# Performance work log

Hardware: AMD Instinct MI355X
Metric: run time of the kernel (lower is better)

The kernel has to match this reference:

```python
import jax, jax.numpy as jnp
import numpy as np

B, S, E, H = 2, 2048, 1024, 16
D = E // H  # head_dim = 64


def _rope_angles(seq_len, d, dtype=jnp.float32):
    # standard RoPE frequencies: theta_i = 10000^{-2i/d}
    inv_freq = 1.0 / (10000.0 ** (jnp.arange(0, d, 2, dtype=dtype) / d))  # [d/2]
    pos = jnp.arange(seq_len, dtype=dtype)                                # [S]
    ang = pos[:, None] * inv_freq[None, :]                                # [S, d/2]
    ang = jnp.concatenate([ang, ang], axis=-1)                            # [S, d]
    return jnp.cos(ang), jnp.sin(ang)


def _rotate_half(t):
    t1, t2 = jnp.split(t, 2, axis=-1)
    return jnp.concatenate([-t2, t1], axis=-1)


def _apply_rope(t, cos, sin):
    # t: [B, H, S, D]; cos/sin: [S, D]
    return t * cos[None, None, :, :] + _rotate_half(t) * sin[None, None, :, :]


def setup_inputs() -> dict:
    key = jax.random.key(0)
    ks = jax.random.split(key, 6)
    x = jax.random.normal(ks[0], (B, S, E), dtype=jnp.float32)
    mask = jnp.tril(jnp.ones((S, S), dtype=bool))  # causal: True = attend
    scale = 1.0 / np.sqrt(E)
    Wq = jax.random.normal(ks[1], (E, E), dtype=jnp.float32) * scale
    Wk = jax.random.normal(ks[2], (E, E), dtype=jnp.float32) * scale
    Wv = jax.random.normal(ks[3], (E, E), dtype=jnp.float32) * scale
    Wo = jax.random.normal(ks[4], (E, E), dtype=jnp.float32) * scale
    z = jnp.zeros((E,), dtype=jnp.float32)
    return {"x": x, "mask": mask, "Wq": Wq, "bq": z, "Wk": Wk, "bk": z,
            "Wv": Wv, "bv": z, "Wo": Wo, "bo": z}


def reference(x, mask, Wq, bq, Wk, bk, Wv, bv, Wo, bo):
    b, s, e = x.shape
    # QKV projections (nn.Linear convention: y = x @ W.T + b)
    def proj(W, bias):
        y = jnp.einsum('bse,fe->bsf', x, W) + bias
        return y.reshape(b, s, H, D).transpose(0, 2, 1, 3)  # [B,H,S,D]
    q, k, v = proj(Wq, bq), proj(Wk, bk), proj(Wv, bv)
    # RoPE on q and k (per-head rotary over head_dim)
    cos, sin = _rope_angles(s, D, dtype=x.dtype)
    q = _apply_rope(q, cos, sin)
    k = _apply_rope(k, cos, sin)
    # SDPA with boolean mask (True = attend)
    scores = jnp.einsum('bhqd,bhkd->bhqk', q, k) / jnp.sqrt(jnp.asarray(D, x.dtype))
    neg = jnp.asarray(jnp.finfo(x.dtype).min, x.dtype)
    scores = jnp.where(mask[None, None, :, :], scores, neg)
    attn = jax.nn.softmax(scores, axis=-1)
    out = jnp.einsum('bhqk,bhkd->bhqd', attn, v)          # [B,H,S,D]
    out = out.transpose(0, 2, 1, 3).reshape(b, s, e)       # [B,S,E]
    return jnp.einsum('bse,fe->bsf', out, Wo) + bo
```

## Files before the change

### kernel.cpp

```cpp
#include <hip/hip_runtime.h>
#include <hip/hip_bf16.h>

typedef unsigned short u16;
typedef unsigned int u32;
typedef __bf16 bf16x8 __attribute__((ext_vector_type(8)));
typedef float f32x4 __attribute__((ext_vector_type(4)));

#define S_LEN 2048
#define NHEAD 16
#define HDIM  64
#define EMB   1024
#define BATCH 2

__device__ __forceinline__ float bf2f(u16 u) {
  union { unsigned int i; float f; } c; c.i = ((unsigned int)u) << 16; return c.f;
}
__device__ __forceinline__ u16 f2bf(float f) {
  union { float f; unsigned int i; } c; c.f = f;
  unsigned int i = c.i;
  return (u16)((i + 0x7FFFu + ((i >> 16) & 1u)) >> 16);
}
__device__ __forceinline__ u16 f2bf_trunc(float f) {
  union { float f; unsigned int i; } c; c.f = f;
  return (u16)(c.i >> 16);
}
__device__ __forceinline__ f32x4 mfma16(bf16x8 a, bf16x8 b, f32x4 c) {
  return __builtin_amdgcn_mfma_f32_16x16x32_bf16(a, b, c, 0, 0, 0);
}
__device__ __forceinline__ void cp16(const u16* g, u16* l) {
  __builtin_amdgcn_global_load_lds(
      (const __attribute__((address_space(1))) u32*)g,
      (__attribute__((address_space(3))) u32*)l, 16, 0, 0);
}

__global__ __launch_bounds__(256) void convert_kernel(
    const void* __restrict__ x, const void* __restrict__ Wq,
    const void* __restrict__ Wk, const void* __restrict__ Wv,
    const void* __restrict__ Wo,
    u16* __restrict__ xb, u16* __restrict__ wqb, u16* __restrict__ wkb,
    u16* __restrict__ wvb, u16* __restrict__ wob,
    int* __restrict__ flag, float2* __restrict__ tab)
{
  __shared__ int s_flag;
  if (threadIdx.x == 0) s_flag = 0;
  __syncthreads();
  {
    const u16* xs = (const u16*)x;
    u16 w0 = xs[threadIdx.x * 2], w1 = xs[threadIdx.x * 2 + 1];
    if ((((w0 >> 7) & 0xFF) >= 0xC0) || (((w1 >> 7) & 0xFF) >= 0xC0))
      atomicOr(&s_flag, 1);
  }
  __syncthreads();
  const int f32io = s_flag;
  if (blockIdx.x == 0 && threadIdx.x == 0) flag[0] = f32io;

  size_t gid = (size_t)blockIdx.x * 256 + threadIdx.x;
  size_t e = gid * 8;
  const void* src; u16* dst; size_t off;
  if (e < 4194304) { src = x; dst = xb; off = e; }
  else {
    size_t rr = e - 4194304;
    int j = (int)(rr >> 20); off = rr & 1048575;
    src = (j == 0) ? Wq : (j == 1) ? Wk : (j == 2) ? Wv : Wo;
    dst = (j == 0) ? wqb : (j == 1) ? wkb : (j == 2) ? wvb : wob;
  }
  if (f32io) {
    const float* s = (const float*)src + off;
    float4 a = *(const float4*)s;
    float4 b2 = *(const float4*)(s + 4);
    ushort4 u0; u0.x = f2bf(a.x); u0.y = f2bf(a.y); u0.z = f2bf(a.z); u0.w = f2bf(a.w);
    ushort4 u1; u1.x = f2bf(b2.x); u1.y = f2bf(b2.y); u1.z = f2bf(b2.z); u1.w = f2bf(b2.w);
    *(ushort4*)(dst + off) = u0;
    *(ushort4*)(dst + off + 4) = u1;
  } else {
    *(uint4*)(dst + off) = *(const uint4*)((const u16*)src + off);
  }

  if (blockIdx.x < 256) {
    int id = blockIdx.x * 256 + threadIdx.x;
    int s = id >> 5, i = id & 31;
    float f = exp2f(-(float)i * 0.41524101186092029f);
    float ang = (float)s * f;
    tab[id] = make_float2(cosf(ang), sinf(ang));
  }
}

__device__ __forceinline__ void gemm_core_db(
    const u16* __restrict__ A, const u16* __restrict__ W,
    int m0, int n0, int t, f32x4 (&acc)[4][4],
    u16* __restrict__ Ash, u16* __restrict__ Bsh)
{
  const int lane = t & 63, lr = lane & 15, quad = lane >> 4;
  const int wv = t >> 6;
  const int wm = (wv & 1) * 64, wn = (wv >> 1) * 64;
  const int r0 = t >> 2;
  const int r1 = (t + 256) >> 2;
  const int c0 = (((t & 3) ^ ((t >> 2) & 3))) * 8;
  const int lds0 = (t & 192) * 8;
  const int lds1 = (256 + (t & 192)) * 8;
  const int qx = ((quad ^ (lr & 3))) * 8;
  const u16* gA0 = A + (size_t)(m0 + r0) * 1024 + c0;
  const u16* gA1 = A + (size_t)(m0 + r1) * 1024 + c0;
  const u16* gB0 = W + (size_t)(n0 + r0) * 1024 + c0;
  const u16* gB1 = W + (size_t)(n0 + r1) * 1024 + c0;

  cp16(gA0, Ash + lds0); cp16(gA1, Ash + lds1);
  cp16(gB0, Bsh + lds0); cp16(gB1, Bsh + lds1);
  __syncthreads();

  for (int kt = 0; kt < 1024; kt += 32) {
    const int cur = (kt >> 5) & 1;
    const u16* Ac = Ash + cur * 4096;
    const u16* Bc = Bsh + cur * 4096;
    bf16x8 af[4], bfr[4];
#pragma unroll
    for (int mi = 0; mi < 4; ++mi)
      af[mi] = *(const bf16x8*)(Ac + (wm + mi * 16 + lr) * 32 + qx);
#pragma unroll
    for (int ni = 0; ni < 4; ++ni)
      bfr[ni] = *(const bf16x8*)(Bc + (wn + ni * 16 + lr) * 32 + qx);
    if (kt + 32 < 1024) {
      u16* An = Ash + (1 - cur) * 4096;
      u16* Bn = Bsh + (1 - cur) * 4096;
      cp16(gA0 + kt + 32, An + lds0); cp16(gA1 + kt + 32, An + lds1);
      cp16(gB0 + kt + 32, Bn + lds0); cp16(gB1 + kt + 32, Bn + lds1);
    }
#pragma unroll
    for (int mi = 0; mi < 4; ++mi)
#pragma unroll
      for (int ni = 0; ni < 4; ++ni)
        acc[mi][ni] = mfma16(af[mi], bfr[ni], acc[mi][ni]);
    __syncthreads();
  }
}

__device__ __forceinline__ void gemm_epilogue(
    int mode, int f32io, f32x4 (&acc)[4][4],
    const void* biasvp, void* outvp, int m0, int n0, int t,
    const float2* __restrict__ tab)
{
  const int lane = t & 63, lr = lane & 15, quad = lane >> 4;
  const int wv = t >> 6;
  const int wm = (wv & 1) * 64, wn = (wv >> 1) * 64;
  const float* biasf = (const float*)biasvp;
  const u16* biasb = (const u16*)biasvp;
#define BIASV(n) (f32io ? biasf[(n)] : bf2f(biasb[(n)]))
  if (mode == 1) {
    u16* Out = (u16*)outvp;
#pragma unroll
    for (int mi = 0; mi < 4; ++mi) {
#pragma unroll
      for (int r = 0; r < 4; ++r) {
        int mm = m0 + wm + mi * 16 + quad * 4 + r;
        int s = mm & (S_LEN - 1), b = mm >> 11;
        float2 cs0 = tab[s * 32 + lr];
        float2 cs1 = tab[s * 32 + 16 + lr];
#pragma unroll
        for (int ni = 0; ni < 4; ++ni) {
          int n = n0 + wn + ni * 16 + lr;
          int h = n >> 6, d = n & 63;
          float v  = acc[mi][ni][r]     + BIASV(n);
          float vp = acc[mi][ni ^ 2][r] + BIASV(n ^ 32);
          float rot = (d < 32) ? -vp : vp;
          float cc = (ni & 1) ? cs1.x : cs0.x;
          float ss = (ni & 1) ? cs1.y : cs0.y;
          size_t off = (((size_t)(b * NHEAD + h)) * S_LEN + s) * HDIM + d;
          Out[off] = f2bf(v * cc + rot * ss);
        }
      }
    }
  } else if (mode == 2) {
    u16* Out = (u16*)outvp;
#pragma unroll
    for (int mi = 0; mi < 4; ++mi) {
      int mm = m0 + wm + mi * 16 + quad * 4;
      int s = mm & (S_LEN - 1), b = mm >> 11;
#pragma unroll
      for (int ni = 0; ni < 4; ++ni) {
        int n = n0 + wn + ni * 16 + lr;
        int h = n >> 6, d = n & 63;
        float bv = BIASV(n);
        u16 p0 = f2bf(acc[mi][ni][0] + bv);
        u16 p1 = f2bf(acc[mi][ni][1] + bv);
        u16 p2 = f2bf(acc[mi][ni][2] + bv);
        u16 p3 = f2bf(acc[mi][ni][3] + bv);
        uint2 pk = make_uint2((u32)p0 | ((u32)p1 << 16),
                              (u32)p2 | ((u32)p3 << 16));
        size_t off = (((size_t)(b * NHEAD + h)) * HDIM + d) * S_LEN + s;
        *(uint2*)(Out + off) = pk;
      }
    }
  }
#undef BIASV
}

__global__ __launch_bounds__(256) void gemm_qkv(
    const u16* __restrict__ A, const u16* __restrict__ Wq,
    const u16* __restrict__ Wk, const u16* __restrict__ Wv,
    const void* bq, const void* bk, const void* bv,
    u16* qo, u16* ko, u16* vo, const int* __restrict__ dflag,
    const float2* __restrict__ tab)
{
  alignas(16) __shared__ u16 Ash[2 * 128 * 32];
  alignas(16) __shared__ u16 Bsh[2 * 128 * 32];
  const int lin = blockIdx.y * 24 + blockIdx.x;
  const int xcd = lin & 7, rr = lin >> 3;
  const int mt = (xcd << 2) + (rr & 3);
  const int nw = rr >> 2;
  const int wsel = nw >> 3;
  const u16* W = (wsel == 0) ? Wq : (wsel == 1) ? Wk : Wv;
  const void* bias = (wsel == 0) ? bq : (wsel == 1) ? bk : bv;
  void* out = (wsel == 0) ? (void*)qo : (wsel == 1) ? (void*)ko : (void*)vo;
  const int mode = (wsel == 2) ? 2 : 1;
  const int m0 = mt * 128, n0 = (nw & 7) * 128;
  f32x4 acc[4][4];
  const f32x4 zero4 = {0.f, 0.f, 0.f, 0.f};
#pragma unroll
  for (int i = 0; i < 4; ++i)
#pragma unroll
    for (int j = 0; j < 4; ++j) acc[i][j] = zero4;
  gemm_core_db(A, W, m0, n0, threadIdx.x, acc, Ash, Bsh);
  gemm_epilogue(mode, dflag[0], acc, bias, out, m0, n0, threadIdx.x, tab);
}

__global__ __launch_bounds__(256) void gemm_out(
    const u16* __restrict__ A, const u16* __restrict__ W,
    const void* bias, void* out, const int* __restrict__ dflag)
{
  alignas(16) __shared__ u16 Ash[2 * 64 * 32];
  alignas(16) __shared__ u16 Bsh[2 * 128 * 32];
  const int t = threadIdx.x, lane = t & 63, wv = t >> 6;
  const int lr = lane & 15, quad = lane >> 4;
  const int lin = blockIdx.y * 8 + blockIdx.x;
  const int xcd = lin & 7, rl = lin >> 3;
  const int mt = (xcd << 3) + (rl & 7);
  const int m0 = mt * 64, n0 = (rl >> 3) * 128;
  const int wm = (wv & 1) * 32, wn = (wv >> 1) * 64;
  const int f32io = dflag[0];

  const int r0 = t >> 2;
  const int r1 = (t + 256) >> 2;
  const int c0 = (((t & 3) ^ ((t >> 2) & 3))) * 8;
  const int lds0 = (t & 192) * 8;
  const int lds1 = (256 + (t & 192)) * 8;
  const int qx = ((quad ^ (lr & 3))) * 8;
  const u16* gA0 = A + (size_t)(m0 + (r0 & 63)) * 1024 + c0;
  const u16* gB0 = W + (size_t)(n0 + r0) * 1024 + c0;
  const u16* gB1 = W + (size_t)(n0 + r1) * 1024 + c0;

  f32x4 acc[2][4];
  const f32x4 zero4 = {0.f, 0.f, 0.f, 0.f};
#pragma unroll
  for (int i = 0; i < 2; ++i)
#pragma unroll
    for (int j = 0; j < 4; ++j) acc[i][j] = zero4;

  cp16(gA0, Ash + lds0);
  cp16(gB0, Bsh + lds0); cp16(gB1, Bsh + lds1);
  __syncthreads();

  for (int kt = 0; kt < 1024; kt += 32) {
    const int cur = (kt >> 5) & 1;
    const u16* Ac = Ash + cur * 2048;
    const u16* Bc = Bsh + cur * 4096;
    bf16x8 af[2], bfr[4];
#pragma unroll
    for (int mi = 0; mi < 2; ++mi)
      af[mi] = *(const bf16x8*)(Ac + (wm + mi * 16 + lr) * 32 + qx);
#pragma unroll
    for (int ni = 0; ni < 4; ++ni)
      bfr[ni] = *(const bf16x8*)(Bc + (wn + ni * 16 + lr) * 32 + qx);
    if (kt + 32 < 1024) {
      u16* An = Ash + (1 - cur) * 2048;
      u16* Bn = Bsh + (1 - cur) * 4096;
      cp16(gA0 + kt + 32, An + lds0);
      cp16(gB0 + kt + 32, Bn + lds0); cp16(gB1 + kt + 32, Bn + lds1);
    }
#pragma unroll
    for (int mi = 0; mi < 2; ++mi)
#pragma unroll
      for (int ni = 0; ni < 4; ++ni)
        acc[mi][ni] = mfma16(af[mi], bfr[ni], acc[mi][ni]);
    __syncthreads();
  }

  const float* biasf = (const float*)bias;
  const u16* biasb = (const u16*)bias;
  float* Outf = (float*)out;
  u16* Outb = (u16*)out;
#pragma unroll
  for (int mi = 0; mi < 2; ++mi) {
#pragma unroll
    for (int r = 0; r < 4; ++r) {
      int mm = m0 + wm + mi * 16 + quad * 4 + r;
#pragma unroll
      for (int ni = 0; ni < 4; ++ni) {
        int n = n0 + wn + ni * 16 + lr;
        float bv = f32io ? biasf[n] : bf2f(biasb[n]);
        float v = acc[mi][ni][r] + bv;
        size_t off = (size_t)mm * 1024 + n;
        if (f32io) Outf[off] = v; else Outb[off] = f2bf(v);
      }
    }
  }
}

__device__ __forceinline__ void attn_phase(
    const bf16x8 (&qf)[2], f32x4 (&oacc)[4], float& lsum,
    const u16 (*__restrict__ Ksh)[72], const u16 (*__restrict__ Vsh)[72],
    u16 (*__restrict__ Pw)[72],
    int kv0, int q0w, bool diag, int lr, int quad)
{
  const f32x4 zero4 = {0.f, 0.f, 0.f, 0.f};
  f32x4 sc[4];
#pragma unroll
  for (int ni = 0; ni < 4; ++ni) {
    bf16x8 kf0 = *(const bf16x8*)&Ksh[ni * 16 + lr][quad * 8];
    bf16x8 kf1 = *(const bf16x8*)&Ksh[ni * 16 + lr][32 + quad * 8];
    f32x4 z = zero4;
    z = mfma16(kf0, qf[0], z);
    z = mfma16(kf1, qf[1], z);
    sc[ni] = z;
  }
  const int qa = q0w + lr;
  if (diag) {
#pragma unroll
    for (int ni = 0; ni < 4; ++ni)
#pragma unroll
      for (int r = 0; r < 4; ++r) {
        float sarg = sc[ni][r] * 0.18033688f - 21.64042561f;
        if (kv0 + ni * 16 + quad * 4 + r > qa) sarg = -1e4f;
        float p = exp2f(sarg);
        sc[ni][r] = p;
        lsum += p;
      }
  } else {
#pragma unroll
    for (int ni = 0; ni < 4; ++ni)
#pragma unroll
      for (int r = 0; r < 4; ++r) {
        float p = exp2f(sc[ni][r] * 0.18033688f - 21.64042561f);
        sc[ni][r] = p;
        lsum += p;
      }
  }
#pragma unroll
  for (int ni = 0; ni < 4; ++ni) {
    u32 lo = (u32)f2bf_trunc(sc[ni][0]) | ((u32)f2bf_trunc(sc[ni][1]) << 16);
    u32 hi = (u32)f2bf_trunc(sc[ni][2]) | ((u32)f2bf_trunc(sc[ni][3]) << 16);
    *(uint2*)&Pw[lr][ni * 16 + quad * 4] = make_uint2(lo, hi);
  }
  bf16x8 pa0 = *(const bf16x8*)&Pw[lr][quad * 8];
  bf16x8 pa1 = *(const bf16x8*)&Pw[lr][32 + quad * 8];
#pragma unroll
  for (int oni = 0; oni < 4; ++oni) {
    bf16x8 vf0 = *(const bf16x8*)&Vsh[oni * 16 + lr][quad * 8];
    bf16x8 vf1 = *(const bf16x8*)&Vsh[oni * 16 + lr][32 + quad * 8];
    oacc[oni] = mfma16(pa0, vf0, oacc[oni]);
    oacc[oni] = mfma16(pa1, vf1, oacc[oni]);
  }
}

__device__ __forceinline__ void attn_phase_half(
    const bf16x8 (&qf)[2], f32x4 (&oacc)[4], float& lsum,
    const u16 (*__restrict__ Ksh)[72], const u16 (*__restrict__ Vsh)[72],
    u16 (*__restrict__ Pw)[72],
    int kv0, int q0w, bool diag, int half, int lr, int quad)
{
  const f32x4 zero4 = {0.f, 0.f, 0.f, 0.f};
  f32x4 sc[2];
#pragma unroll
  for (int i = 0; i < 2; ++i) {
    const int ni = half * 2 + i;
    bf16x8 kf0 = *(const bf16x8*)&Ksh[ni * 16 + lr][quad * 8];
    bf16x8 kf1 = *(const bf16x8*)&Ksh[ni * 16 + lr][32 + quad * 8];
    f32x4 z = zero4;
    z = mfma16(kf0, qf[0], z);
    z = mfma16(kf1, qf[1], z);
    sc[i] = z;
  }
  const int qa = q0w + lr;
  if (diag) {
#pragma unroll
    for (int i = 0; i < 2; ++i)
#pragma unroll
      for (int r = 0; r < 4; ++r) {
        float sarg = sc[i][r] * 0.18033688f - 21.64042561f;
        if (kv0 + (half * 2 + i) * 16 + quad * 4 + r > qa) sarg = -1e4f;
        float p = exp2f(sarg);
        sc[i][r] = p;
        lsum += p;
      }
  } else {
#pragma unroll
    for (int i = 0; i < 2; ++i)
#pragma unroll
      for (int r = 0; r < 4; ++r) {
        float p = exp2f(sc[i][r] * 0.18033688f - 21.64042561f);
        sc[i][r] = p;
        lsum += p;
      }
  }
#pragma unroll
  for (int i = 0; i < 2; ++i) {
    u32 lo = (u32)f2bf_trunc(sc[i][0]) | ((u32)f2bf_trunc(sc[i][1]) << 16);
    u32 hi = (u32)f2bf_trunc(sc[i][2]) | ((u32)f2bf_trunc(sc[i][3]) << 16);
    *(uint2*)&Pw[lr][(half * 2 + i) * 16 + quad * 4] = make_uint2(lo, hi);
  }
  bf16x8 pa = *(const bf16x8*)&Pw[lr][half * 32 + quad * 8];
#pragma unroll
  for (int oni = 0; oni < 4; ++oni) {
    bf16x8 vf = *(const bf16x8*)&Vsh[oni * 16 + lr][half * 32 + quad * 8];
    oacc[oni] = mfma16(pa, vf, oacc[oni]);
  }
}

__device__ __forceinline__ void attn_finish(
    f32x4 (&oacc)[4], float lsum, u16* __restrict__ O,
    int bh, int q0w, int lr, int quad)
{
  const int b = bh >> 4, h = bh & 15;
  lsum += __shfl_xor(lsum, 16);
  lsum += __shfl_xor(lsum, 32);
  const float inv = 1.f / lsum;
#pragma unroll
  for (int r = 0; r < 4; ++r) {
    const float scale = __shfl(inv, quad * 4 + r);
#pragma unroll
    for (int oni = 0; oni < 4; ++oni) {
      int s = q0w + quad * 4 + r;
      int e = h * HDIM + oni * 16 + lr;
      O[((size_t)(b * S_LEN + s)) * EMB + e] = f2bf(oacc[oni][r] * scale);
    }
  }
}

__global__ __launch_bounds__(512, 4) void attn_kernel(
    const u16* __restrict__ Q, const u16* __restrict__ Kr,
    const u16* __restrict__ Vt, u16* __restrict__ O)
{
  alignas(16) __shared__ u16 Kdb[2][64][72];
  alignas(16) __shared__ u16 Vdb[2][64][72];
  alignas(16) __shared__ u16 Psh[8][16][72];
  const int t = threadIdx.x, lane = t & 63, wv = t >> 6;
  const int lr = lane & 15, quad = lane >> 4;
  const int lin = blockIdx.y * 16 + blockIdx.x;
  const int xcd = lin & 7, rl = lin >> 3;
  const int bh = (xcd << 2) + (rl & 3);
  const int qtA = rl >> 2;
  const int qtB = 31 - qtA;
  const bool grpA = (wv < 4);
  const int q0own = (grpA ? qtA : qtB) * 64 + (wv & 3) * 16;
  const int q0B = qtB * 64 + (wv & 3) * 16;
  const size_t base = (size_t)bh * S_LEN * HDIM;

  bf16x8 qfO[2], qfH[2];
  {
    const u16* qrow = Q + base + (size_t)(q0own + lr) * HDIM + quad * 8;
    qfO[0] = *(const bf16x8*)qrow;
    qfO[1] = *(const bf16x8*)(qrow + 32);
  }
  if (grpA) {
    const u16* qrow = Q + base + (size_t)(q0B + lr) * HDIM + quad * 8;
    qfH[0] = *(const bf16x8*)qrow;
    qfH[1] = *(const bf16x8*)(qrow + 32);
  } else { qfH[0] = qfO[0]; qfH[1] = qfO[1]; }

  f32x4 oacc0[4], oacc1[4];
  float lsum0 = 0.f, lsum1 = 0.f;
  const f32x4 zero4 = {0.f, 0.f, 0.f, 0.f};
#pragma unroll
  for (int i = 0; i < 4; ++i) { oacc0[i] = zero4; oacc1[i] = zero4; }

  const int rr = t >> 3, cc = (t & 7) * 8;
  uint4 krg = *(const uint4*)(Kr + base + (size_t)rr * HDIM + cc);
  uint4 vrg = *(const uint4*)(Vt + base + (size_t)rr * S_LEN + cc);

  for (int j = 0; j <= qtB; ++j) {
    const int cur = j & 1;
    *(uint4*)&Kdb[cur][rr][cc] = krg;
    *(uint4*)&Vdb[cur][rr][cc] = vrg;
    __syncthreads();
    if (j < qtB) {
      const int kv1 = (j + 1) * 64;
      krg = *(const uint4*)(Kr + base + (size_t)(kv1 + rr) * HDIM + cc);
      vrg = *(const uint4*)(Vt + base + (size_t)rr * S_LEN + kv1 + cc);
    }
    if (j <= qtA) {
      attn_phase(qfO, oacc0, lsum0, Kdb[cur], Vdb[cur], Psh[wv],
                 j * 64, q0own, grpA && (j == qtA), lr, quad);
    } else if (grpA) {
      attn_phase_half(qfH, oacc1, lsum1, Kdb[cur], Vdb[cur], Psh[wv],
                      j * 64, q0B, j == qtB, 1, lr, quad);
    } else {
      attn_phase_half(qfO, oacc0, lsum0, Kdb[cur], Vdb[cur], Psh[wv],
                      j * 64, q0B, j == qtB, 0, lr, quad);
    }
  }

  __syncthreads();
  if (grpA) {
    float* dst = (float*)&Psh[0][0][0] + (size_t)(wv * 64 + lane) * 17;
#pragma unroll
    for (int oni = 0; oni < 4; ++oni)
#pragma unroll
      for (int r = 0; r < 4; ++r) dst[oni * 4 + r] = oacc1[oni][r];
    dst[16] = lsum1;
  }
  __syncthreads();
  if (!grpA) {
    const float* src =
        (const float*)&Psh[0][0][0] + (size_t)((wv - 4) * 64 + lane) * 17;
#pragma unroll
    for (int oni = 0; oni < 4; ++oni)
#pragma unroll
      for (int r = 0; r < 4; ++r) oacc0[oni][r] += src[oni * 4 + r];
    lsum0 += src[16];
  }
  attn_finish(oacc0, lsum0, O, bh, q0own, lr, quad);
}

extern "C" void kernel_launch(void* const* d_in, const int* in_sizes, int n_in,
                              void* d_out, int out_size, void* d_ws, size_t ws_size,
                              hipStream_t stream) {
  const void* x  = d_in[0];
  const void* Wq = d_in[2]; const void* bq = d_in[3];
  const void* Wk = d_in[4]; const void* bk = d_in[5];
  const void* Wv = d_in[6]; const void* bv = d_in[7];
  const void* Wo = d_in[8]; const void* bo = d_in[9];

  char* ws = (char*)d_ws;
  int* flag = (int*)ws;
  u16* xb  = (u16*)(ws + 256);
  u16* qws = xb  + 4194304;
  u16* kws = qws + 4194304;
  u16* vws = kws + 4194304;
  u16* wqb = vws + 4194304;
  u16* wkb = wqb + 1048576;
  u16* wvb = wkb + 1048576;
  u16* wob = wvb + 1048576;
  float2* tab = (float2*)(wob + 1048576);
  u16* ows = xb;

  convert_kernel<<<4096, 256, 0, stream>>>(x, Wq, Wk, Wv, Wo,
                                           xb, wqb, wkb, wvb, wob, flag, tab);
  gemm_qkv<<<dim3(24, 32), 256, 0, stream>>>(xb, wqb, wkb, wvb,
                                             bq, bk, bv, qws, kws, vws, flag, tab);
  attn_kernel<<<dim3(16, 32), 512, 0, stream>>>(qws, kws, vws, ows);
  gemm_out<<<dim3(8, 64), 256, 0, stream>>>(ows, wob, bo, d_out, flag);
}
```

Before: 202.4 us.

## Have each attention wave own two query tiles and hoist GEMM prefetch issue

Attention blocks shrink from 8 waves to 4, with each wave processing both the early (A) and late (B) query tiles. Each K/V tile loaded to shared memory is reused for two query sets within one wave, which removes the split-half balancing path and the cross-wave reduction through shared memory at the end. In both GEMM loops, the async global-to-LDS prefetch is now issued before the fragment reads from shared memory so the copies start earlier. The trade-off is higher register pressure per wave, fewer waves per block to hide latency, and each thread now loads twice as much K/V per tile.

Measured after the change: 215.2 us. 1.06x slower.

```diff
diff --git a/kernel.cpp b/kernel.cpp
--- a/kernel.cpp
+++ b/kernel.cpp
@@ -112,19 +112,19 @@
     const int cur = (kt >> 5) & 1;
     const u16* Ac = Ash + cur * 4096;
     const u16* Bc = Bsh + cur * 4096;
-    bf16x8 af[4], bfr[4];
-#pragma unroll
-    for (int mi = 0; mi < 4; ++mi)
-      af[mi] = *(const bf16x8*)(Ac + (wm + mi * 16 + lr) * 32 + qx);
-#pragma unroll
-    for (int ni = 0; ni < 4; ++ni)
-      bfr[ni] = *(const bf16x8*)(Bc + (wn + ni * 16 + lr) * 32 + qx);
     if (kt + 32 < 1024) {
       u16* An = Ash + (1 - cur) * 4096;
       u16* Bn = Bsh + (1 - cur) * 4096;
       cp16(gA0 + kt + 32, An + lds0); cp16(gA1 + kt + 32, An + lds1);
       cp16(gB0 + kt + 32, Bn + lds0); cp16(gB1 + kt + 32, Bn + lds1);
     }
+    bf16x8 af[4], bfr[4];
+#pragma unroll
+    for (int mi = 0; mi < 4; ++mi)
+      af[mi] = *(const bf16x8*)(Ac + (wm + mi * 16 + lr) * 32 + qx);
+#pragma unroll
+    for (int ni = 0; ni < 4; ++ni)
+      bfr[ni] = *(const bf16x8*)(Bc + (wn + ni * 16 + lr) * 32 + qx);
 #pragma unroll
     for (int mi = 0; mi < 4; ++mi)
 #pragma unroll
@@ -263,19 +263,19 @@
     const int cur = (kt >> 5) & 1;
     const u16* Ac = Ash + cur * 2048;
     const u16* Bc = Bsh + cur * 4096;
-    bf16x8 af[2], bfr[4];
-#pragma unroll
-    for (int mi = 0; mi < 2; ++mi)
-      af[mi] = *(const bf16x8*)(Ac + (wm + mi * 16 + lr) * 32 + qx);
-#pragma unroll
-    for (int ni = 0; ni < 4; ++ni)
-      bfr[ni] = *(const bf16x8*)(Bc + (wn + ni * 16 + lr) * 32 + qx);
     if (kt + 32 < 1024) {
       u16* An = Ash + (1 - cur) * 2048;
       u16* Bn = Bsh + (1 - cur) * 4096;
       cp16(gA0 + kt + 32, An + lds0);
       cp16(gB0 + kt + 32, Bn + lds0); cp16(gB1 + kt + 32, Bn + lds1);
     }
+    bf16x8 af[2], bfr[4];
+#pragma unroll
+    for (int mi = 0; mi < 2; ++mi)
+      af[mi] = *(const bf16x8*)(Ac + (wm + mi * 16 + lr) * 32 + qx);
+#pragma unroll
+    for (int ni = 0; ni < 4; ++ni)
+      bfr[ni] = *(const bf16x8*)(Bc + (wn + ni * 16 + lr) * 32 + qx);
 #pragma unroll
     for (int mi = 0; mi < 2; ++mi)
 #pragma unroll
@@ -302,6 +302,82 @@
         if (f32io) Outf[off] = v; else Outb[off] = f2bf(v);
       }
     }
+  }
+}
+
+__device__ __forceinline__ void attn_phase_dual(
+    const bf16x8 (&qfA)[2], const bf16x8 (&qfB)[2],
+    f32x4 (&oaccA)[4], f32x4 (&oaccB)[4], float& lsumA, float& lsumB,
+    const u16 (*__restrict__ Ksh)[72], const u16 (*__restrict__ Vsh)[72],
+    u16 (*__restrict__ PwA)[72], u16 (*__restrict__ PwB)[72],
+    int kv0, int q0A, bool diagA, int lr, int quad)
+{
+  const f32x4 zero4 = {0.f, 0.f, 0.f, 0.f};
+  f32x4 scA[4], scB[4];
+#pragma unroll
+  for (int ni = 0; ni < 4; ++ni) {
+    bf16x8 kf0 = *(const bf16x8*)&Ksh[ni * 16 + lr][quad * 8];
+    bf16x8 kf1 = *(const bf16x8*)&Ksh[ni * 16 + lr][32 + quad * 8];
+    f32x4 zA = zero4;
+    zA = mfma16(kf0, qfA[0], zA);
+    zA = mfma16(kf1, qfA[1], zA);
+    scA[ni] = zA;
+    f32x4 zB = zero4;
+    zB = mfma16(kf0, qfB[0], zB);
+    zB = mfma16(kf1, qfB[1], zB);
+    scB[ni] = zB;
+  }
+  const int qa = q0A + lr;
+  if (diagA) {
+#pragma unroll
+    for (int ni = 0; ni < 4; ++ni)
+#pragma unroll
+      for (int r = 0; r < 4; ++r) {
+        float sarg = scA[ni][r] * 0.18033688f - 21.64042561f;
+        if (kv0 + ni * 16 + quad * 4 + r > qa) sarg = -1e4f;
+        float p = exp2f(sarg);
+        scA[ni][r] = p;
+        lsumA += p;
+      }
+  } else {
+#pragma unroll
+    for (int ni = 0; ni < 4; ++ni)
+#pragma unroll
+      for (int r = 0; r < 4; ++r) {
+        float p = exp2f(scA[ni][r] * 0.18033688f - 21.64042561f);
+        scA[ni][r] = p;
+        lsumA += p;
+      }
+  }
+#pragma unroll
+  for (int ni = 0; ni < 4; ++ni)
+#pragma unroll
+    for (int r = 0; r < 4; ++r) {
+      float p = exp2f(scB[ni][r] * 0.18033688f - 21.64042561f);
+      scB[ni][r] = p;
+      lsumB += p;
+    }
+#pragma unroll
+  for (int ni = 0; ni < 4; ++ni) {
+    u32 lo = (u32)f2bf_trunc(scA[ni][0]) | ((u32)f2bf_trunc(scA[ni][1]) << 16);
+    u32 hi = (u32)f2bf_trunc(scA[ni][2]) | ((u32)f2bf_trunc(scA[ni][3]) << 16);
+    *(uint2*)&PwA[lr][ni * 16 + quad * 4] = make_uint2(lo, hi);
+    u32 lo2 = (u32)f2bf_trunc(scB[ni][0]) | ((u32)f2bf_trunc(scB[ni][1]) << 16);
+    u32 hi2 = (u32)f2bf_trunc(scB[ni][2]) | ((u32)f2bf_trunc(scB[ni][3]) << 16);
+    *(uint2*)&PwB[lr][ni * 16 + quad * 4] = make_uint2(lo2, hi2);
+  }
+  bf16x8 paA0 = *(const bf16x8*)&PwA[lr][quad * 8];
+  bf16x8 paA1 = *(const bf16x8*)&PwA[lr][32 + quad * 8];
+  bf16x8 paB0 = *(const bf16x8*)&PwB[lr][quad * 8];
+  bf16x8 paB1 = *(const bf16x8*)&PwB[lr][32 + quad * 8];
+#pragma unroll
+  for (int oni = 0; oni < 4; ++oni) {
+    bf16x8 vf0 = *(const bf16x8*)&Vsh[oni * 16 + lr][quad * 8];
+    bf16x8 vf1 = *(const bf16x8*)&Vsh[oni * 16 + lr][32 + quad * 8];
+    oaccA[oni] = mfma16(paA0, vf0, oaccA[oni]);
+    oaccA[oni] = mfma16(paA1, vf1, oaccA[oni]);
+    oaccB[oni] = mfma16(paB0, vf0, oaccB[oni]);
+    oaccB[oni] = mfma16(paB1, vf1, oaccB[oni]);
   }
 }
 
@@ -361,60 +437,6 @@
   }
 }
 
-__device__ __forceinline__ void attn_phase_half(
-    const bf16x8 (&qf)[2], f32x4 (&oacc)[4], float& lsum,
-    const u16 (*__restrict__ Ksh)[72], const u16 (*__restrict__ Vsh)[72],
-    u16 (*__restrict__ Pw)[72],
-    int kv0, int q0w, bool diag, int half, int lr, int quad)
-{
-  const f32x4 zero4 = {0.f, 0.f, 0.f, 0.f};
-  f32x4 sc[2];
-#pragma unroll
-  for (int i = 0; i < 2; ++i) {
-    const int ni = half * 2 + i;
-    bf16x8 kf0 = *(const bf16x8*)&Ksh[ni * 16 + lr][quad * 8];
-    bf16x8 kf1 = *(const bf16x8*)&Ksh[ni * 16 + lr][32 + quad * 8];
-    f32x4 z = zero4;
-    z = mfma16(kf0, qf[0], z);
-    z = mfma16(kf1, qf[1], z);
-    sc[i] = z;
-  }
-  const int qa = q0w + lr;
-  if (diag) {
-#pragma unroll
-    for (int i = 0; i < 2; ++i)
-#pragma unroll
-      for (int r = 0; r < 4; ++r) {
-        float sarg = sc[i][r] * 0.18033688f - 21.64042561f;
-        if (kv0 + (half * 2 + i) * 16 + quad * 4 + r > qa) sarg = -1e4f;
-        float p = exp2f(sarg);
-        sc[i][r] = p;
-        lsum += p;
-      }
-  } else {
-#pragma unroll
-    for (int i = 0; i < 2; ++i)
-#pragma unroll
-      for (int r = 0; r < 4; ++r) {
-        float p = exp2f(sc[i][r] * 0.18033688f - 21.64042561f);
-        sc[i][r] = p;
-        lsum += p;
-      }
-  }
-#pragma unroll
-  for (int i = 0; i < 2; ++i) {
-    u32 lo = (u32)f2bf_trunc(sc[i][0]) | ((u32)f2bf_trunc(sc[i][1]) << 16);
-    u32 hi = (u32)f2bf_trunc(sc[i][2]) | ((u32)f2bf_trunc(sc[i][3]) << 16);
-    *(uint2*)&Pw[lr][(half * 2 + i) * 16 + quad * 4] = make_uint2(lo, hi);
-  }
-  bf16x8 pa = *(const bf16x8*)&Pw[lr][half * 32 + quad * 8];
-#pragma unroll
-  for (int oni = 0; oni < 4; ++oni) {
-    bf16x8 vf = *(const bf16x8*)&Vsh[oni * 16 + lr][half * 32 + quad * 8];
-    oacc[oni] = mfma16(pa, vf, oacc[oni]);
-  }
-}
-
 __device__ __forceinline__ void attn_finish(
     f32x4 (&oacc)[4], float lsum, u16* __restrict__ O,
     int bh, int q0w, int lr, int quad)
@@ -435,13 +457,14 @@
   }
 }
 
-__global__ __launch_bounds__(512, 4) void attn_kernel(
+__global__ __launch_bounds__(256) void attn_kernel(
     const u16* __restrict__ Q, const u16* __restrict__ Kr,
     const u16* __restrict__ Vt, u16* __restrict__ O)
 {
   alignas(16) __shared__ u16 Kdb[2][64][72];
   alignas(16) __shared__ u16 Vdb[2][64][72];
-  alignas(16) __shared__ u16 Psh[8][16][72];
+  alignas(16) __shared__ u16 PshA[4][16][72];
+  alignas(16) __shared__ u16 PshB[4][16][72];
   const int t = threadIdx.x, lane = t & 63, wv = t >> 6;
   const int lr = lane & 15, quad = lane >> 4;
   const int lin = blockIdx.y * 16 + blockIdx.x;
@@ -449,75 +472,60 @@
   const int bh = (xcd << 2) + (rl & 3);
   const int qtA = rl >> 2;
   const int qtB = 31 - qtA;
-  const bool grpA = (wv < 4);
-  const int q0own = (grpA ? qtA : qtB) * 64 + (wv & 3) * 16;
-  const int q0B = qtB * 64 + (wv & 3) * 16;
+  const int q0A = qtA * 64 + wv * 16;
+  const int q0B = qtB * 64 + wv * 16;
   const size_t base = (size_t)bh * S_LEN * HDIM;
 
-  bf16x8 qfO[2], qfH[2];
+  bf16x8 qfA[2], qfB[2];
   {
-    const u16* qrow = Q + base + (size_t)(q0own + lr) * HDIM + quad * 8;
-    qfO[0] = *(const bf16x8*)qrow;
-    qfO[1] = *(const bf16x8*)(qrow + 32);
-  }
-  if (grpA) {
+    const u16* qrow = Q + base + (size_t)(q0A + lr) * HDIM + quad * 8;
+    qfA[0] = *(const bf16x8*)qrow;
+    qfA[1] = *(const bf16x8*)(qrow + 32);
+  }
+  {
     const u16* qrow = Q + base + (size_t)(q0B + lr) * HDIM + quad * 8;
-    qfH[0] = *(const bf16x8*)qrow;
-    qfH[1] = *(const bf16x8*)(qrow + 32);
-  } else { qfH[0] = qfO[0]; qfH[1] = qfO[1]; }
-
-  f32x4 oacc0[4], oacc1[4];
-  float lsum0 = 0.f, lsum1 = 0.f;
+    qfB[0] = *(const bf16x8*)qrow;
+    qfB[1] = *(const bf16x8*)(qrow + 32);
+  }
+
+  f32x4 oaccA[4], oaccB[4];
+  float lsumA = 0.f, lsumB = 0.f;
   const f32x4 zero4 = {0.f, 0.f, 0.f, 0.f};
 #pragma unroll
-  for (int i = 0; i < 4; ++i) { oacc0[i] = zero4; oacc1[i] = zero4; }
-
-  const int rr = t >> 3, cc = (t & 7) * 8;
-  uint4 krg = *(const uint4*)(Kr + base + (size_t)rr * HDIM + cc);
-  uint4 vrg = *(const uint4*)(Vt + base + (size_t)rr * S_LEN + cc);
+  for (int i = 0; i < 4; ++i) { oaccA[i] = zero4; oaccB[i] = zero4; }
+
+  const int rr = t >> 2, cc = (t & 3) * 8;
+  uint4 krg0 = *(const uint4*)(Kr + base + (size_t)rr * HDIM + cc);
+  uint4 krg1 = *(const uint4*)(Kr + base + (size_t)rr * HDIM + cc + 32);
+  uint4 vrg0 = *(const uint4*)(Vt + base + (size_t)rr * S_LEN + cc);
+  uint4 vrg1 = *(const uint4*)(Vt + base + (size_t)rr * S_LEN + cc + 32);
 
   for (int j = 0; j <= qtB; ++j) {
     const int cur = j & 1;
-    *(uint4*)&Kdb[cur][rr][cc] = krg;
-    *(uint4*)&Vdb[cur][rr][cc] = vrg;
+    *(uint4*)&Kdb[cur][rr][cc] = krg0;
+    *(uint4*)&Kdb[cur][rr][cc + 32] = krg1;
+    *(uint4*)&Vdb[cur][rr][cc] = vrg0;
+    *(uint4*)&Vdb[cur][rr][cc + 32] = vrg1;
     __syncthreads();
     if (j < qtB) {
       const int kv1 = (j + 1) * 64;
-      krg = *(const uint4*)(Kr + base + (size_t)(kv1 + rr) * HDIM + cc);
-      vrg = *(const uint4*)(Vt + base + (size_t)rr * S_LEN + kv1 + cc);
+      krg0 = *(const uint4*)(Kr + base + (size_t)(kv1 + rr) * HDIM + cc);
+      krg1 = *(const uint4*)(Kr + base + (size_t)(kv1 + rr) * HDIM + cc + 32);
+      vrg0 = *(const uint4*)(Vt + base + (size_t)rr * S_LEN + kv1 + cc);
+      vrg1 = *(const uint4*)(Vt + base + (size_t)rr * S_LEN + kv1 + cc + 32);
     }
     if (j <= qtA) {
-      attn_phase(qfO, oacc0, lsum0, Kdb[cur], Vdb[cur], Psh[wv],
-                 j * 64, q0own, grpA && (j == qtA), lr, quad);
-    } else if (grpA) {
-      attn_phase_half(qfH, oacc1, lsum1, Kdb[cur], Vdb[cur], Psh[wv],
-                      j * 64, q0B, j == qtB, 1, lr, quad);
+      attn_phase_dual(qfA, qfB, oaccA, oaccB, lsumA, lsumB,
+                      Kdb[cur], Vdb[cur], PshA[wv], PshB[wv],
+                      j * 64, q0A, j == qtA, lr, quad);
     } else {
-      attn_phase_half(qfO, oacc0, lsum0, Kdb[cur], Vdb[cur], Psh[wv],
-                      j * 64, q0B, j == qtB, 0, lr, quad);
-    }
-  }
-
-  __syncthreads();
-  if (grpA) {
-    float* dst = (float*)&Psh[0][0][0] + (size_t)(wv * 64 + lane) * 17;
-#pragma unroll
-    for (int oni = 0; oni < 4; ++oni)
-#pragma unroll
-      for (int r = 0; r < 4; ++r) dst[oni * 4 + r] = oacc1[oni][r];
-    dst[16] = lsum1;
-  }
-  __syncthreads();
-  if (!grpA) {
-    const float* src =
-        (const float*)&Psh[0][0][0] + (size_t)((wv - 4) * 64 + lane) * 17;
-#pragma unroll
-    for (int oni = 0; oni < 4; ++oni)
-#pragma unroll
-      for (int r = 0; r < 4; ++r) oacc0[oni][r] += src[oni * 4 + r];
-    lsum0 += src[16];
-  }
-  attn_finish(oacc0, lsum0, O, bh, q0own, lr, quad);
+      attn_phase(qfB, oaccB, lsumB, Kdb[cur], Vdb[cur], PshB[wv],
+                 j * 64, q0B, j == qtB, lr, quad);
+    }
+  }
+
+  attn_finish(oaccA, lsumA, O, bh, q0A, lr, quad);
+  attn_finish(oaccB, lsumB, O, bh, q0B, lr, quad);
 }
 
 extern "C" void kernel_launch(void* const* d_in, const int* in_sizes, int n_in,
@@ -546,6 +554,6 @@
                                            xb, wqb, wkb, wvb, wob, flag, tab);
   gemm_qkv<<<dim3(24, 32), 256, 0, stream>>>(xb, wqb, wkb, wvb,
                                              bq, bk, bv, qws, kws, vws, flag, tab);
-  attn_kernel<<<dim3(16, 32), 512, 0, stream>>>(qws, kws, vws, ows);
+  attn_kernel<<<dim3(16, 32), 256, 0, stream>>>(qws, kws, vws, ows);
   gemm_out<<<dim3(8, 64), 256, 0, stream>>>(ows, wob, bo, d_out, flag);
 }
```

## Split attention KV tiles by half across wave groups for both query tiles

Applied to the files above, without the earlier changes.

Attention work is redistributed so that each wave group handles one half of every KV tile for both paired query tiles (A and B), sharing K/V fragment loads across two query blocks. Before, wave groups owned whole tiles of different queries. A cross-group reduction in LDS then combines the partial accumulators and row sums, and only the lower group writes output. The GEMM loops also issue next-tile async copies before reading LDS fragments. This raises register pressure and doubles the P scratch buffers, and the final reduction moves more data.

After: 211.7 us. 4.6% more time.

```diff
diff --git a/kernel.cpp b/kernel.cpp
--- a/kernel.cpp
+++ b/kernel.cpp
@@ -112,19 +112,19 @@
     const int cur = (kt >> 5) & 1;
     const u16* Ac = Ash + cur * 4096;
     const u16* Bc = Bsh + cur * 4096;
-    bf16x8 af[4], bfr[4];
-#pragma unroll
-    for (int mi = 0; mi < 4; ++mi)
-      af[mi] = *(const bf16x8*)(Ac + (wm + mi * 16 + lr) * 32 + qx);
-#pragma unroll
-    for (int ni = 0; ni < 4; ++ni)
-      bfr[ni] = *(const bf16x8*)(Bc + (wn + ni * 16 + lr) * 32 + qx);
     if (kt + 32 < 1024) {
       u16* An = Ash + (1 - cur) * 4096;
       u16* Bn = Bsh + (1 - cur) * 4096;
       cp16(gA0 + kt + 32, An + lds0); cp16(gA1 + kt + 32, An + lds1);
       cp16(gB0 + kt + 32, Bn + lds0); cp16(gB1 + kt + 32, Bn + lds1);
     }
+    bf16x8 af[4], bfr[4];
+#pragma unroll
+    for (int mi = 0; mi < 4; ++mi)
+      af[mi] = *(const bf16x8*)(Ac + (wm + mi * 16 + lr) * 32 + qx);
+#pragma unroll
+    for (int ni = 0; ni < 4; ++ni)
+      bfr[ni] = *(const bf16x8*)(Bc + (wn + ni * 16 + lr) * 32 + qx);
 #pragma unroll
     for (int mi = 0; mi < 4; ++mi)
 #pragma unroll
@@ -263,19 +263,19 @@
     const int cur = (kt >> 5) & 1;
     const u16* Ac = Ash + cur * 2048;
     const u16* Bc = Bsh + cur * 4096;
-    bf16x8 af[2], bfr[4];
-#pragma unroll
-    for (int mi = 0; mi < 2; ++mi)
-      af[mi] = *(const bf16x8*)(Ac + (wm + mi * 16 + lr) * 32 + qx);
-#pragma unroll
-    for (int ni = 0; ni < 4; ++ni)
-      bfr[ni] = *(const bf16x8*)(Bc + (wn + ni * 16 + lr) * 32 + qx);
     if (kt + 32 < 1024) {
       u16* An = Ash + (1 - cur) * 2048;
       u16* Bn = Bsh + (1 - cur) * 4096;
       cp16(gA0 + kt + 32, An + lds0);
       cp16(gB0 + kt + 32, Bn + lds0); cp16(gB1 + kt + 32, Bn + lds1);
     }
+    bf16x8 af[2], bfr[4];
+#pragma unroll
+    for (int mi = 0; mi < 2; ++mi)
+      af[mi] = *(const bf16x8*)(Ac + (wm + mi * 16 + lr) * 32 + qx);
+#pragma unroll
+    for (int ni = 0; ni < 4; ++ni)
+      bfr[ni] = *(const bf16x8*)(Bc + (wn + ni * 16 + lr) * 32 + qx);
 #pragma unroll
     for (int mi = 0; mi < 2; ++mi)
 #pragma unroll
@@ -305,59 +305,76 @@
   }
 }
 
-__device__ __forceinline__ void attn_phase(
-    const bf16x8 (&qf)[2], f32x4 (&oacc)[4], float& lsum,
+__device__ __forceinline__ void attn_phase_dual_half(
+    const bf16x8 (&qfA)[2], const bf16x8 (&qfB)[2],
+    f32x4 (&oaccA)[4], f32x4 (&oaccB)[4], float& lsumA, float& lsumB,
     const u16 (*__restrict__ Ksh)[72], const u16 (*__restrict__ Vsh)[72],
-    u16 (*__restrict__ Pw)[72],
-    int kv0, int q0w, bool diag, int lr, int quad)
+    u16 (*__restrict__ PwA)[72], u16 (*__restrict__ PwB)[72],
+    int kv0, int q0A, bool diagA, int half, int lr, int quad)
 {
   const f32x4 zero4 = {0.f, 0.f, 0.f, 0.f};
-  f32x4 sc[4];
-#pragma unroll
-  for (int ni = 0; ni < 4; ++ni) {
+  f32x4 scA[2], scB[2];
+#pragma unroll
+  for (int i = 0; i < 2; ++i) {
+    const int ni = half * 2 + i;
     bf16x8 kf0 = *(const bf16x8*)&Ksh[ni * 16 + lr][quad * 8];
     bf16x8 kf1 = *(const bf16x8*)&Ksh[ni * 16 + lr][32 + quad * 8];
-    f32x4 z = zero4;
-    z = mfma16(kf0, qf[0], z);
-    z = mfma16(kf1, qf[1], z);
-    sc[ni] = z;
-  }
-  const int qa = q0w + lr;
-  if (diag) {
-#pragma unroll
-    for (int ni = 0; ni < 4; ++ni)
-#pragma unroll
-      for (int r = 0; r < 4; ++r) {
-        float sarg = sc[ni][r] * 0.18033688f - 21.64042561f;
-        if (kv0 + ni * 16 + quad * 4 + r > qa) sarg = -1e4f;
+    f32x4 zA = zero4;
+    zA = mfma16(kf0, qfA[0], zA);
+    zA = mfma16(kf1, qfA[1], zA);
+    scA[i] = zA;
+    f32x4 zB = zero4;
+    zB = mfma16(kf0, qfB[0], zB);
+    zB = mfma16(kf1, qfB[1], zB);
+    scB[i] = zB;
+  }
+  const int qa = q0A + lr;
+  if (diagA) {
+#pragma unroll
+    for (int i = 0; i < 2; ++i)
+#pragma unroll
+      for (int r = 0; r < 4; ++r) {
+        float sarg = scA[i][r] * 0.18033688f - 21.64042561f;
+        if (kv0 + (half * 2 + i) * 16 + quad * 4 + r > qa) sarg = -1e4f;
         float p = exp2f(sarg);
-        sc[ni][r] = p;
-        lsum += p;
+        scA[i][r] = p;
+        lsumA += p;
       }
   } else {
 #pragma unroll
-    for (int ni = 0; ni < 4; ++ni)
-#pragma unroll
-      for (int r = 0; r < 4; ++r) {
-        float p = exp2f(sc[ni][r] * 0.18033688f - 21.64042561f);
-        sc[ni][r] = p;
-        lsum += p;
-      }
-  }
-#pragma unroll
-  for (int ni = 0; ni < 4; ++ni) {
-    u32 lo = (u32)f2bf_trunc(sc[ni][0]) | ((u32)f2bf_trunc(sc[ni][1]) << 16);
-    u32 hi = (u32)f2bf_trunc(sc[ni][2]) | ((u32)f2bf_trunc(sc[ni][3]) << 16);
-    *(uint2*)&Pw[lr][ni * 16 + quad * 4] = make_uint2(lo, hi);
-  }
-  bf16x8 pa0 = *(const bf16x8*)&Pw[lr][quad * 8];
-  bf16x8 pa1 = *(const bf16x8*)&Pw[lr][32 + quad * 8];
+    for (int i = 0; i < 2; ++i)
+#pragma unroll
+      for (int r = 0; r < 4; ++r) {
+        float p = exp2f(scA[i][r] * 0.18033688f - 21.64042561f);
+        scA[i][r] = p;
+        lsumA += p;
+      }
+  }
+#pragma unroll
+  for (int i = 0; i < 2; ++i)
+#pragma unroll
+    for (int r = 0; r < 4; ++r) {
+      float p = exp2f(scB[i][r] * 0.18033688f - 21.64042561f);
+      scB[i][r] = p;
+      lsumB += p;
+    }
+#pragma unroll
+  for (int i = 0; i < 2; ++i) {
+    const int col = (half * 2 + i) * 16 + quad * 4;
+    u32 loA = (u32)f2bf_trunc(scA[i][0]) | ((u32)f2bf_trunc(scA[i][1]) << 16);
+    u32 hiA = (u32)f2bf_trunc(scA[i][2]) | ((u32)f2bf_trunc(scA[i][3]) << 16);
+    *(uint2*)&PwA[lr][col] = make_uint2(loA, hiA);
+    u32 loB = (u32)f2bf_trunc(scB[i][0]) | ((u32)f2bf_trunc(scB[i][1]) << 16);
+    u32 hiB = (u32)f2bf_trunc(scB[i][2]) | ((u32)f2bf_trunc(scB[i][3]) << 16);
+    *(uint2*)&PwB[lr][col] = make_uint2(loB, hiB);
+  }
+  bf16x8 paA = *(const bf16x8*)&PwA[lr][half * 32 + quad * 8];
+  bf16x8 paB = *(const bf16x8*)&PwB[lr][half * 32 + quad * 8];
 #pragma unroll
   for (int oni = 0; oni < 4; ++oni) {
-    bf16x8 vf0 = *(const bf16x8*)&Vsh[oni * 16 + lr][quad * 8];
-    bf16x8 vf1 = *(const bf16x8*)&Vsh[oni * 16 + lr][32 + quad * 8];
-    oacc[oni] = mfma16(pa0, vf0, oacc[oni]);
-    oacc[oni] = mfma16(pa1, vf1, oacc[oni]);
+    bf16x8 vf = *(const bf16x8*)&Vsh[oni * 16 + lr][half * 32 + quad * 8];
+    oaccA[oni] = mfma16(paA, vf, oaccA[oni]);
+    oaccB[oni] = mfma16(paB, vf, oaccB[oni]);
   }
 }
 
@@ -439,9 +456,11 @@
     const u16* __restrict__ Q, const u16* __restrict__ Kr,
     const u16* __restrict__ Vt, u16* __restrict__ O)
 {
-  alignas(16) __shared__ u16 Kdb[2][64][72];
-  alignas(16) __shared__ u16 Vdb[2][64][72];
-  alignas(16) __shared__ u16 Psh[8][16][72];
+  alignas(16) __shared__ u16 SH[36864];
+  u16 (*Kdb)[64][72] = reinterpret_cast<u16(*)[64][72]>(SH);
+  u16 (*Vdb)[64][72] = reinterpret_cast<u16(*)[64][72]>(SH + 9216);
+  u16 (*PA)[16][72] = reinterpret_cast<u16(*)[16][72]>(SH + 18432);
+  u16 (*PB)[16][72] = reinterpret_cast<u16(*)[16][72]>(SH + 27648);
   const int t = threadIdx.x, lane = t & 63, wv = t >> 6;
   const int lr = lane & 15, quad = lane >> 4;
   const int lin = blockIdx.y * 16 + blockIdx.x;
@@ -449,28 +468,28 @@
   const int bh = (xcd << 2) + (rl & 3);
   const int qtA = rl >> 2;
   const int qtB = 31 - qtA;
-  const bool grpA = (wv < 4);
-  const int q0own = (grpA ? qtA : qtB) * 64 + (wv & 3) * 16;
+  const int half = wv >> 2;
+  const int q0A = qtA * 64 + (wv & 3) * 16;
   const int q0B = qtB * 64 + (wv & 3) * 16;
   const size_t base = (size_t)bh * S_LEN * HDIM;
 
-  bf16x8 qfO[2], qfH[2];
+  bf16x8 qfA[2], qfB[2];
   {
-    const u16* qrow = Q + base + (size_t)(q0own + lr) * HDIM + quad * 8;
-    qfO[0] = *(const bf16x8*)qrow;
-    qfO[1] = *(const bf16x8*)(qrow + 32);
-  }
-  if (grpA) {
+    const u16* qrow = Q + base + (size_t)(q0A + lr) * HDIM + quad * 8;
+    qfA[0] = *(const bf16x8*)qrow;
+    qfA[1] = *(const bf16x8*)(qrow + 32);
+  }
+  {
     const u16* qrow = Q + base + (size_t)(q0B + lr) * HDIM + quad * 8;
-    qfH[0] = *(const bf16x8*)qrow;
-    qfH[1] = *(const bf16x8*)(qrow + 32);
-  } else { qfH[0] = qfO[0]; qfH[1] = qfO[1]; }
-
-  f32x4 oacc0[4], oacc1[4];
-  float lsum0 = 0.f, lsum1 = 0.f;
+    qfB[0] = *(const bf16x8*)qrow;
+    qfB[1] = *(const bf16x8*)(qrow + 32);
+  }
+
+  f32x4 oaccA[4], oaccB[4];
+  float lsumA = 0.f, lsumB = 0.f;
   const f32x4 zero4 = {0.f, 0.f, 0.f, 0.f};
 #pragma unroll
-  for (int i = 0; i < 4; ++i) { oacc0[i] = zero4; oacc1[i] = zero4; }
+  for (int i = 0; i < 4; ++i) { oaccA[i] = zero4; oaccB[i] = zero4; }
 
   const int rr = t >> 3, cc = (t & 7) * 8;
   uint4 krg = *(const uint4*)(Kr + base + (size_t)rr * HDIM + cc);
@@ -487,37 +506,42 @@
       vrg = *(const uint4*)(Vt + base + (size_t)rr * S_LEN + kv1 + cc);
     }
     if (j <= qtA) {
-      attn_phase(qfO, oacc0, lsum0, Kdb[cur], Vdb[cur], Psh[wv],
-                 j * 64, q0own, grpA && (j == qtA), lr, quad);
-    } else if (grpA) {
-      attn_phase_half(qfH, oacc1, lsum1, Kdb[cur], Vdb[cur], Psh[wv],
-                      j * 64, q0B, j == qtB, 1, lr, quad);
+      attn_phase_dual_half(qfA, qfB, oaccA, oaccB, lsumA, lsumB,
+                           Kdb[cur], Vdb[cur], PA[wv], PB[wv],
+                           j * 64, q0A, j == qtA, half, lr, quad);
     } else {
-      attn_phase_half(qfO, oacc0, lsum0, Kdb[cur], Vdb[cur], Psh[wv],
-                      j * 64, q0B, j == qtB, 0, lr, quad);
+      attn_phase_half(qfB, oaccB, lsumB, Kdb[cur], Vdb[cur], PB[wv],
+                      j * 64, q0B, j == qtB, half, lr, quad);
     }
   }
 
   __syncthreads();
-  if (grpA) {
-    float* dst = (float*)&Psh[0][0][0] + (size_t)(wv * 64 + lane) * 17;
+  float* scm = (float*)&SH[0];
+  if (half) {
+    float* d = scm + (size_t)((wv - 4) * 64 + lane) * 34;
 #pragma unroll
     for (int oni = 0; oni < 4; ++oni)
 #pragma unroll
-      for (int r = 0; r < 4; ++r) dst[oni * 4 + r] = oacc1[oni][r];
-    dst[16] = lsum1;
+      for (int r = 0; r < 4; ++r) {
+        d[oni * 4 + r] = oaccA[oni][r];
+        d[16 + oni * 4 + r] = oaccB[oni][r];
+      }
+    d[32] = lsumA; d[33] = lsumB;
   }
   __syncthreads();
-  if (!grpA) {
-    const float* src =
-        (const float*)&Psh[0][0][0] + (size_t)((wv - 4) * 64 + lane) * 17;
+  if (!half) {
+    const float* s = scm + (size_t)(wv * 64 + lane) * 34;
 #pragma unroll
     for (int oni = 0; oni < 4; ++oni)
 #pragma unroll
-      for (int r = 0; r < 4; ++r) oacc0[oni][r] += src[oni * 4 + r];
-    lsum0 += src[16];
-  }
-  attn_finish(oacc0, lsum0, O, bh, q0own, lr, quad);
+      for (int r = 0; r < 4; ++r) {
+        oaccA[oni][r] += s[oni * 4 + r];
+        oaccB[oni][r] += s[16 + oni * 4 + r];
+      }
+    lsumA += s[32]; lsumB += s[33];
+    attn_finish(oaccA, lsumA, O, bh, q0A, lr, quad);
+    attn_finish(oaccB, lsumB, O, bh, q0B, lr, quad);
+  }
 }
 
 extern "C" void kernel_launch(void* const* d_in, const int* in_sizes, int n_in,
```
